# Kernel optimization log

Measured on AMD Instinct MI355X. Metric: run time of the kernel, lower is better.

## Reference

```python
import jax, jax.numpy as jnp
import numpy as np

GC_ALPHA = 3.0  # saturation factor in MTGNN-style graph constructor
TOP_K = 5       # ctor arg: GraphConstructor(n_classes, 5, dim)
EPS_NORM = 1e-12


def setup_inputs() -> dict:
    key = jax.random.key(0)
    k1, k2, k3, k4, k5 = jax.random.split(key, 5)
    B, C, H, W = 32, 384, 80, 80
    N = 27
    return {
        "x": jax.random.normal(k1, (B, C, H, W), dtype=jnp.float32),
        "alpha": jnp.ones((), dtype=jnp.float32),
        "clusters": jax.random.normal(k2, (N, C), dtype=jnp.float32),
        "gc_w1": jax.random.normal(k3, (C, C), dtype=jnp.float32) / np.sqrt(C),
        "gc_w2": jax.random.normal(k4, (C, C), dtype=jnp.float32) / np.sqrt(C),
        "gcn_w": jax.random.normal(k5, (C, C), dtype=jnp.float32) / np.sqrt(C),
    }


def _refine_clusters(clusters, gc_w1, gc_w2, gcn_w):
    # GraphConstructor: learned asymmetric adjacency over n_classes nodes, top-k sparsified
    n = clusters.shape[0]
    a = jnp.tanh(GC_ALPHA * (clusters @ gc_w1))          # [n, d]
    b = jnp.tanh(GC_ALPHA * (clusters @ gc_w2))          # [n, d]
    adj = jax.nn.relu(jnp.tanh(GC_ALPHA * (a @ b.T - b @ a.T)))  # [n, n]
    topv, _ = jax.lax.top_k(adj, TOP_K)
    A = jnp.where(adj >= topv[:, -1:], adj, 0.0)         # keep top-k per row
    # GCNConv (no bias): add self-loops, symmetric normalization
    A_hat = A + jnp.eye(n, dtype=A.dtype)
    dinv = 1.0 / jnp.sqrt(A_hat.sum(axis=1))
    A_norm = dinv[:, None] * A_hat * dinv[None, :]
    return A_norm @ (clusters @ gcn_w)                   # [n, d]


def reference(x, alpha, clusters, gc_w1, gc_w2, gcn_w):
    # mp=True path: refine codebook with tiny GCN over learned graph
    cl = _refine_clusters(clusters, gc_w1, gc_w2, gcn_w)
    # cosine similarity of per-pixel features against codebook
    nc = cl / jnp.maximum(jnp.linalg.norm(cl, axis=1, keepdims=True), EPS_NORM)
    nf = x / jnp.maximum(jnp.linalg.norm(x, axis=1, keepdims=True), EPS_NORM)
    inner_products = jnp.einsum('bchw,nc->bnhw', nf, nc)          # [B, n, H, W]
    cluster_probs = jax.nn.softmax(inner_products * alpha, axis=1)
    cluster_loss = -(cluster_probs * inner_products).sum(axis=1).mean()
    # entropy over unnormalized similarities (computed in original forward)
    p = jax.nn.softmax(jnp.einsum('bchw,nc->bnhw', x, clusters), axis=1)
    entropy = (-(p * jnp.log(p + 1e-10)).sum(axis=1)).mean()
    return cluster_loss, inner_products, cl, entropy
```

## Files before the change

### kernel.cpp

```cpp
#include <hip/hip_runtime.h>
#include <math.h>

#define N_CL   27
#define C_DIM  384
#define HW_SZ  6400
#define B_SZ   32
#define NPIX   (B_SZ*HW_SZ)
#define NTILE  3200
#define NCHUNK 12
#define WSF_PARTS 24576
#define ENT_OFF (1 + (size_t)NPIX*N_CL + (size_t)N_CL*C_DIM)

typedef unsigned short ushort_t;
using bf16x8 = __attribute__((ext_vector_type(8))) short;
using f32x4  = __attribute__((ext_vector_type(4))) float;

__device__ __forceinline__ float xla_tanh_f32(float x) {
    const float c = 7.99881172180175781f;
    if (fabsf(x) < 0.0004f) return x;
    const float xc = fminf(fmaxf(x, -c), c);
    const float x2 = xc*xc;
    float p = fmaf(x2, -2.76076847742355e-16f, 2.00018790482477e-13f);
    p = fmaf(x2, p, -8.60467152213735e-11f);
    p = fmaf(x2, p,  5.12229709037114e-08f);
    p = fmaf(x2, p,  1.48572235717979e-05f);
    p = fmaf(x2, p,  6.37261928875436e-04f);
    p = fmaf(x2, p,  4.89352455891786e-03f);
    p = xc*p;
    float q = fmaf(x2, 1.19825839466702e-06f, 1.18534705686654e-04f);
    q = fmaf(x2, q, 2.26843463243900e-03f);
    q = fmaf(x2, q, 4.89352518554385e-03f);
    return p/q;
}

__global__ __launch_bounds__(384) void cl_refine_mm(const float* __restrict__ clusters,
                                                    const float* __restrict__ w1,
                                                    const float* __restrict__ w2,
                                                    const float* __restrict__ w3,
                                                    float* __restrict__ ws) {
    const int i = blockIdx.x;
    const int m = blockIdx.y;
    const int j = threadIdx.x;
    __shared__ float crow[C_DIM];
    crow[j] = clusters[i*C_DIM + j];
    __syncthreads();
    const float* __restrict__ W = (m==0) ? w1 : (m==1) ? w2 : w3;
    float s0=0.f,s1=0.f,s2=0.f,s3=0.f;
    #pragma unroll 4
    for (int k=0;k<C_DIM;k+=4){
        s0 = fmaf(crow[k+0], W[(size_t)(k+0)*C_DIM + j], s0);
        s1 = fmaf(crow[k+1], W[(size_t)(k+1)*C_DIM + j], s1);
        s2 = fmaf(crow[k+2], W[(size_t)(k+2)*C_DIM + j], s2);
        s3 = fmaf(crow[k+3], W[(size_t)(k+3)*C_DIM + j], s3);
    }
    const float acc = (s0+s1)+(s2+s3);
    ws[(size_t)m*N_CL*C_DIM + i*C_DIM + j] = (m<2) ? xla_tanh_f32(3.0f*acc) : acc;
}

__global__ __launch_bounds__(1024) void cl_adj_graph(float* ws,
                                                     const float* __restrict__ clusters_g,
                                                     float* __restrict__ out) {
    const float* cg = ws + 2*N_CL*C_DIM;
    float* cl_out = out + 1 + (size_t)NPIX*N_CL;
    const int t = threadIdx.x;

    __shared__ float Ash[N_CL][C_DIM+1];
    __shared__ float Bsh[N_CL][C_DIM+1];
    __shared__ float anorm[N_CL][N_CL+1];
    __shared__ float dinv[N_CL];
    __shared__ float rinv[N_CL];
    __shared__ float cls[N_CL][C_DIM];

    for (int idx=t; idx<N_CL*C_DIM; idx+=1024){
        const int i = idx / C_DIM, k = idx - i*C_DIM;
        Ash[i][k] = ws[idx];
        Bsh[i][k] = ws[N_CL*C_DIM + idx];
    }
    __syncthreads();
    if (t < N_CL*N_CL) {
        const int i = t / N_CL, j = t - (t / N_CL)*N_CL;
        float p0=0,p1=0,p2=0,p3=0,q0=0,q1=0,q2=0,q3=0;
        for (int k=0;k<C_DIM;k+=4){
            p0=fmaf(Ash[i][k+0],Bsh[j][k+0],p0); p1=fmaf(Ash[i][k+1],Bsh[j][k+1],p1);
            p2=fmaf(Ash[i][k+2],Bsh[j][k+2],p2); p3=fmaf(Ash[i][k+3],Bsh[j][k+3],p3);
            q0=fmaf(Bsh[i][k+0],Ash[j][k+0],q0); q1=fmaf(Bsh[i][k+1],Ash[j][k+1],q1);
            q2=fmaf(Bsh[i][k+2],Ash[j][k+2],q2); q3=fmaf(Bsh[i][k+3],Ash[j][k+3],q3);
        }
        const float s1v=(p0+p1)+(p2+p3), s2v=(q0+q1)+(q2+q3);
        anorm[i][j] = fmaxf(xla_tanh_f32(3.0f*(s1v-s2v)), 0.f);
    }
    __syncthreads();
    if (t < N_CL) {
        unsigned mask=0; float thr=0.f;
        for (int s=0;s<5;s++){
            float bv=-1.f; int bi2=0;
            for (int j=0;j<N_CL;j++){
                if (mask & (1u<<j)) continue;
                const float v = anorm[t][j];
                if (v > bv){ bv=v; bi2=j; }
            }
            mask |= 1u<<bi2; thr = bv;
        }
        float rs=0.f;
        for (int j=0;j<N_CL;j++){
            float v = anorm[t][j];
            v = (v >= thr) ? v : 0.f;
            if (j==t) v += 1.f;
            anorm[t][j] = v;
            rs += v;
        }
        dinv[t] = 1.0f / sqrtf(rs);
    }
    __syncthreads();
    if (t < N_CL*N_CL) {
        const int i = t / N_CL, j = t - (t / N_CL)*N_CL;
        anorm[i][j] = dinv[i]*anorm[i][j]*dinv[j];
    }
    __syncthreads();
    for (int idx=t; idx<N_CL*C_DIM; idx+=1024){
        const int i = idx / C_DIM, d = idx - i*C_DIM;
        float s=0.f;
        #pragma unroll
        for (int j=0;j<N_CL;j++) s = fmaf(anorm[i][j], cg[(size_t)j*C_DIM + d], s);
        cls[i][d] = s;
        cl_out[idx] = s;
    }
    __syncthreads();
    if (t < N_CL) {
        float ssq=0.f;
        for (int d=0; d<C_DIM; d++){ const float v=cls[t][d]; ssq=fmaf(v,v,ssq); }
        rinv[t] = 1.0f / fmaxf(sqrtf(ssq), 1e-12f);
    }
    __syncthreads();
    ushort_t* wpk = (ushort_t*)ws;
    for (int idx=t; idx<64*C_DIM; idx+=1024){
        const int n = idx / C_DIM, k = idx - n*C_DIM;
        float v = 0.f;
        if (n < N_CL) v = cls[n][k] * rinv[n];
        else if (n >= 32 && n < 32+N_CL) v = clusters_g[(size_t)(n-32)*C_DIM + k];
        const unsigned bits = __float_as_uint(v);
        const ushort_t hi = (ushort_t)(bits >> 16);
        const float lof = v - __uint_as_float(bits & 0xFFFF0000u);
        const ushort_t lo = (ushort_t)(__float_as_uint(lof) >> 16);
        wpk[idx] = hi;
        wpk[64*C_DIM + idx] = lo;
    }
}

__global__ __launch_bounds__(256, 5) void cl_mfma(const float* __restrict__ x,
                                                  const float* __restrict__ alpha_p,
                                                  const ushort_t* __restrict__ wpk,
                                                  float* __restrict__ ws,
                                                  float* __restrict__ out) {
    __shared__ __align__(16) ushort_t lB[2][2][64][40];
    __shared__ float redL[4], redE[4];

    const int tid = threadIdx.x;
    const int blk = blockIdx.x;
    const int b   = blk / 100;
    const int hw0 = (blk - b*100) * 64;
    const float* __restrict__ xb = x + (size_t)b*C_DIM*HW_SZ + hw0;

    const int lane = tid & 63;
    const int w    = tid >> 6;
    const int l15  = lane & 15;
    const int g    = lane >> 4;
    const int k0   = g*8;
    const float* __restrict__ xl = xb + (w*16 + l15);

    const int b_n  = tid >> 2;
    const int b_kb = (tid & 3) * 8;

    uint4 rb0, rb1;
    #define LOADB(c) {                                                            \
        rb0 = *(const uint4*)(wpk + (size_t)(     b_n)*C_DIM + (c)*32 + b_kb);    \
        rb1 = *(const uint4*)(wpk + (size_t)(64 + b_n)*C_DIM + (c)*32 + b_kb); }
    #define WRITEB(bf) {                                                          \
        *(uint4*)(&lB[bf][0][b_n][b_kb]) = rb0;                                   \
        *(uint4*)(&lB[bf][1][b_n][b_kb]) = rb1; }

    #define LOADA(c, S) {                                                         \
        const float* pA = xl + (size_t)((c)*32 + k0)*HW_SZ;                       \
        R##S##0 = pA[0*HW_SZ]; R##S##1 = pA[1*HW_SZ];                             \
        R##S##2 = pA[2*HW_SZ]; R##S##3 = pA[3*HW_SZ];                             \
        R##S##4 = pA[4*HW_SZ]; R##S##5 = pA[5*HW_SZ];                             \
        R##S##6 = pA[6*HW_SZ]; R##S##7 = pA[7*HW_SZ]; }

    union { ushort_t u[8]; bf16x8 v; } Ah;
    float ss = 0.f;
    #define CVT1(e, R) {                                                          \
        Ah.u[e] = (ushort_t)(__float_as_uint(R) >> 16);                           \
        ss = fmaf(R, R, ss); }
    #define CONVERT(S) {                                                          \
        CVT1(0,R##S##0) CVT1(1,R##S##1) CVT1(2,R##S##2) CVT1(3,R##S##3)           \
        CVT1(4,R##S##4) CVT1(5,R##S##5) CVT1(6,R##S##6) CVT1(7,R##S##7) }

    f32x4 acc0={0,0,0,0}, acc1={0,0,0,0}, acc2={0,0,0,0}, acc3={0,0,0,0};
    #define DOMFMA(cur) {                                                         \
        _Pragma("unroll")                                                         \
        for (int t = 0; t < 4; t++) {                                             \
            union { uint4 q; bf16x8 v; } Bh, Bl;                                  \
            Bh.q = *(const uint4*)(&lB[cur][0][t*16 + l15][k0]);                  \
            Bl.q = *(const uint4*)(&lB[cur][1][t*16 + l15][k0]);                  \
            f32x4 a = (t==0)?acc0:(t==1)?acc1:(t==2)?acc2:acc3;                   \
            a = __builtin_amdgcn_mfma_f32_16x16x32_bf16(Ah.v, Bh.v, a, 0,0,0);    \
            a = __builtin_amdgcn_mfma_f32_16x16x32_bf16(Ah.v, Bl.v, a, 0,0,0);    \
            if (t==0) acc0=a; else if (t==1) acc1=a; else if (t==2) acc2=a;       \
            else acc3=a;                                                          \
        } }

    #define KBAR() { asm volatile("s_waitcnt lgkmcnt(0)" ::: "memory");           \
                     __builtin_amdgcn_s_barrier(); }

    float Ra0,Ra1,Ra2,Ra3,Ra4,Ra5,Ra6,Ra7;
    float Rb0,Rb1,Rb2,Rb3,Rb4,Rb5,Rb6,Rb7;
    float Rc0,Rc1,Rc2,Rc3,Rc4,Rc5,Rc6,Rc7;
    float Rd0,Rd1,Rd2,Rd3,Rd4,Rd5,Rd6,Rd7;

    LOADB(0); WRITEB(0);
    LOADB(1);
    LOADA(0, a);
    LOADA(1, b);
    LOADA(2, c);
    LOADA(3, d);
    KBAR();

    #define STEP(cc, S, p) {                                                      \
        CONVERT(S);                                                               \
        DOMFMA(p);                                                                \
        if ((cc)+1 < NCHUNK) WRITEB((p)^1);                                       \
        if ((cc)+2 < NCHUNK) LOADB((cc)+2);                                       \
        if ((cc)+4 < NCHUNK) LOADA((cc)+4, S);                                    \
        if ((cc)+1 < NCHUNK) KBAR(); }

    STEP(0,a,0)  STEP(1,b,1)  STEP(2,c,0)  STEP(3,d,1)
    STEP(4,a,0)  STEP(5,b,1)  STEP(6,c,0)  STEP(7,d,1)
    STEP(8,a,0)  STEP(9,b,1)  STEP(10,c,0) STEP(11,d,1)

    ss += __shfl_xor(ss, 16);
    ss += __shfl_xor(ss, 32);
    f32x4 invv;
    #pragma unroll
    for (int r = 0; r < 4; r++) {
        const float s2 = __shfl(ss, g*4 + r);
        invv[r] = 1.0f / fmaxf(sqrtf(s2), 1e-12f);
    }

    const float alpha = alpha_p[0];
    float* __restrict__ out1 = out + 1;
    const int pxb = hw0 + w*16 + g*4;

    f32x4 st0, st1;
    #pragma unroll
    for (int r=0;r<4;r++){ st0[r] = acc0[r]*invv[r]; st1[r] = acc1[r]*invv[r]; }
    *(f32x4*)(out1 + (size_t)b*N_CL*HW_SZ + (size_t)l15*HW_SZ + pxb) = st0;
    if (l15 <= 10)
        *(f32x4*)(out1 + (size_t)b*N_CL*HW_SZ + (size_t)(16+l15)*HW_SZ + pxb) = st1;

    float wloss = 0.f, went = 0.f;
    #pragma unroll
    for (int r=0;r<4;r++){
        const float ip0 = st0[r], ip1 = st1[r];
        const float v0 = alpha*ip0;
        const float v1 = (l15<=10) ? alpha*ip1 : -INFINITY;
        float mx = fmaxf(v0, v1);
        #pragma unroll
        for (int m=1;m<16;m<<=1) mx = fmaxf(mx, __shfl_xor(mx, m));
        const float e0 = expf(v0 - mx);
        const float e1 = (l15<=10) ? expf(v1 - mx) : 0.f;
        float z = e0 + e1;
        float tt = fmaf(e0, ip0, (l15<=10) ? e1*ip1 : 0.f);
        #pragma unroll
        for (int m=1;m<16;m<<=1){ z += __shfl_xor(z,m); tt += __shfl_xor(tt,m); }
        wloss += tt/z;
        const float c0 = acc2[r];
        const float c1 = (l15<=10) ? acc3[r] : -INFINITY;
        float emx = fmaxf(c0, c1);
        #pragma unroll
        for (int m=1;m<16;m<<=1) emx = fmaxf(emx, __shfl_xor(emx, m));
        const float f0 = expf(c0 - emx);
        const float f1 = (l15<=10) ? expf(c1 - emx) : 0.f;
        float ez = f0 + f1;
        #pragma unroll
        for (int m=1;m<16;m<<=1) ez += __shfl_xor(ez,m);
        const float iz = 1.0f/ez;
        const float p0 = f0*iz, p1 = f1*iz;
        float te = -p0*logf(p0+1e-10f) - p1*logf(p1+1e-10f);
        #pragma unroll
        for (int m=1;m<16;m<<=1) te += __shfl_xor(te,m);
        went += te;
    }
    wloss += __shfl_xor(wloss,16); wloss += __shfl_xor(wloss,32);
    went  += __shfl_xor(went ,16); went  += __shfl_xor(went ,32);
    if (lane == 0) { redL[w] = wloss; redE[w] = went; }
    __syncthreads();
    if (tid == 0) {
        float* parts = ws + WSF_PARTS;
        parts[blk]         = redL[0]+redL[1]+redL[2]+redL[3];
        parts[NTILE + blk] = redE[0]+redE[1]+redE[2]+redE[3];
    }
}

__global__ __launch_bounds__(1024) void cl_final_reduce(const float* __restrict__ ws,
                                                        float* __restrict__ out) {
    __shared__ float r[1024];
    const int t = threadIdx.x;
    const float* parts = ws + WSF_PARTS;
    float s = 0.f;
    for (int j=t; j<NTILE; j+=1024) s += parts[j];
    r[t] = s; __syncthreads();
    for (int sft=512;sft>0;sft>>=1){ if (t<sft) r[t]+=r[t+sft]; __syncthreads(); }
    if (t==0) out[0] = -r[0]*(1.0f/NPIX);
    __syncthreads();
    s = 0.f;
    for (int j=t; j<NTILE; j+=1024) s += parts[NTILE + j];
    r[t] = s; __syncthreads();
    for (int sft=512;sft>0;sft>>=1){ if (t<sft) r[t]+=r[t+sft]; __syncthreads(); }
    if (t==0) out[ENT_OFF] = r[0]*(1.0f/NPIX);
}

extern "C" void kernel_launch(void* const* d_in, const int* in_sizes, int n_in,
                              void* d_out, int out_size, void* d_ws, size_t ws_size,
                              hipStream_t stream) {
    const float* x        = (const float*)d_in[0];
    const float* alpha    = (const float*)d_in[1];
    const float* clusters = (const float*)d_in[2];
    const float* w1       = (const float*)d_in[3];
    const float* w2       = (const float*)d_in[4];
    const float* w3       = (const float*)d_in[5];
    float* out = (float*)d_out;
    float* ws  = (float*)d_ws;

    cl_refine_mm<<<dim3(27,3), dim3(384), 0, stream>>>(clusters, w1, w2, w3, ws);
    cl_adj_graph<<<dim3(1), dim3(1024), 0, stream>>>(ws, clusters, out);
    cl_mfma<<<dim3(NTILE), dim3(256), 0, stream>>>(x, alpha, (const ushort_t*)ws, ws, out);
    cl_final_reduce<<<dim3(1), dim3(1024), 0, stream>>>(ws, out);
}
```

Before: 159.9 us.

## Double pixel tile per block to reuse codebook LDS loads across two fragments

Each block now covers 128 pixels instead of 64, and each wave computes two 16-pixel MFMA fragments that share the same B (codebook) fragments read from LDS. This halves the block count and the per-pixel cost of B staging and barriers. The A prefetch depth drops from four chunks to two chunks across two fragments, and the occupancy hint goes from 5 to 4 waves, which trades latency hiding for more register accumulators.

New measurement: 153.2 us. 4.2% less time.

```diff
diff --git a/kernel.cpp b/kernel.cpp
--- a/kernel.cpp
+++ b/kernel.cpp
@@ -6,7 +6,7 @@
 #define HW_SZ  6400
 #define B_SZ   32
 #define NPIX   (B_SZ*HW_SZ)
-#define NTILE  3200
+#define NTILE  1600
 #define NCHUNK 12
 #define WSF_PARTS 24576
 #define ENT_OFF (1 + (size_t)NPIX*N_CL + (size_t)N_CL*C_DIM)
@@ -147,7 +147,7 @@
     }
 }
 
-__global__ __launch_bounds__(256, 5) void cl_mfma(const float* __restrict__ x,
+__global__ __launch_bounds__(256, 4) void cl_mfma(const float* __restrict__ x,
                                                   const float* __restrict__ alpha_p,
                                                   const ushort_t* __restrict__ wpk,
                                                   float* __restrict__ ws,
@@ -157,8 +157,8 @@
 
     const int tid = threadIdx.x;
     const int blk = blockIdx.x;
-    const int b   = blk / 100;
-    const int hw0 = (blk - b*100) * 64;
+    const int b   = blk / 50;
+    const int hw0 = (blk - b*50) * 128;
     const float* __restrict__ xb = x + (size_t)b*C_DIM*HW_SZ + hw0;
 
     const int lane = tid & 63;
@@ -166,7 +166,8 @@
     const int l15  = lane & 15;
     const int g    = lane >> 4;
     const int k0   = g*8;
-    const float* __restrict__ xl = xb + (w*16 + l15);
+    const float* __restrict__ xl0 = xb + (w*32 + l15);
+    const float* __restrict__ xl1 = xl0 + 16;
 
     const int b_n  = tid >> 2;
     const int b_kb = (tid & 3) * 8;
@@ -179,34 +180,42 @@
         *(uint4*)(&lB[bf][0][b_n][b_kb]) = rb0;                                   \
         *(uint4*)(&lB[bf][1][b_n][b_kb]) = rb1; }
 
-    #define LOADA(c, S) {                                                         \
-        const float* pA = xl + (size_t)((c)*32 + k0)*HW_SZ;                       \
+    #define LOADA(c, S, XL) {                                                     \
+        const float* pA = (XL) + (size_t)((c)*32 + k0)*HW_SZ;                     \
         R##S##0 = pA[0*HW_SZ]; R##S##1 = pA[1*HW_SZ];                             \
         R##S##2 = pA[2*HW_SZ]; R##S##3 = pA[3*HW_SZ];                             \
         R##S##4 = pA[4*HW_SZ]; R##S##5 = pA[5*HW_SZ];                             \
         R##S##6 = pA[6*HW_SZ]; R##S##7 = pA[7*HW_SZ]; }
 
-    union { ushort_t u[8]; bf16x8 v; } Ah;
-    float ss = 0.f;
-    #define CVT1(e, R) {                                                          \
-        Ah.u[e] = (ushort_t)(__float_as_uint(R) >> 16);                           \
-        ss = fmaf(R, R, ss); }
-    #define CONVERT(S) {                                                          \
+    union { ushort_t u[8]; bf16x8 v; } A0h, A1h;
+    float ss0 = 0.f, ss1 = 0.f;
+    #define CVT0(e, R) { A0h.u[e] = (ushort_t)(__float_as_uint(R) >> 16);         \
+                         ss0 = fmaf(R, R, ss0); }
+    #define CVT1(e, R) { A1h.u[e] = (ushort_t)(__float_as_uint(R) >> 16);         \
+                         ss1 = fmaf(R, R, ss1); }
+    #define CONVERT0(S) {                                                         \
+        CVT0(0,R##S##0) CVT0(1,R##S##1) CVT0(2,R##S##2) CVT0(3,R##S##3)           \
+        CVT0(4,R##S##4) CVT0(5,R##S##5) CVT0(6,R##S##6) CVT0(7,R##S##7) }
+    #define CONVERT1(S) {                                                         \
         CVT1(0,R##S##0) CVT1(1,R##S##1) CVT1(2,R##S##2) CVT1(3,R##S##3)           \
         CVT1(4,R##S##4) CVT1(5,R##S##5) CVT1(6,R##S##6) CVT1(7,R##S##7) }
 
-    f32x4 acc0={0,0,0,0}, acc1={0,0,0,0}, acc2={0,0,0,0}, acc3={0,0,0,0};
-    #define DOMFMA(cur) {                                                         \
+    f32x4 acc00={0,0,0,0}, acc01={0,0,0,0}, acc02={0,0,0,0}, acc03={0,0,0,0};
+    f32x4 acc10={0,0,0,0}, acc11={0,0,0,0}, acc12={0,0,0,0}, acc13={0,0,0,0};
+    #define DOCHUNK(p) {                                                          \
         _Pragma("unroll")                                                         \
         for (int t = 0; t < 4; t++) {                                             \
             union { uint4 q; bf16x8 v; } Bh, Bl;                                  \
-            Bh.q = *(const uint4*)(&lB[cur][0][t*16 + l15][k0]);                  \
-            Bl.q = *(const uint4*)(&lB[cur][1][t*16 + l15][k0]);                  \
-            f32x4 a = (t==0)?acc0:(t==1)?acc1:(t==2)?acc2:acc3;                   \
-            a = __builtin_amdgcn_mfma_f32_16x16x32_bf16(Ah.v, Bh.v, a, 0,0,0);    \
-            a = __builtin_amdgcn_mfma_f32_16x16x32_bf16(Ah.v, Bl.v, a, 0,0,0);    \
-            if (t==0) acc0=a; else if (t==1) acc1=a; else if (t==2) acc2=a;       \
-            else acc3=a;                                                          \
+            Bh.q = *(const uint4*)(&lB[p][0][t*16 + l15][k0]);                    \
+            Bl.q = *(const uint4*)(&lB[p][1][t*16 + l15][k0]);                    \
+            f32x4 a0 = (t==0)?acc00:(t==1)?acc01:(t==2)?acc02:acc03;              \
+            f32x4 a1 = (t==0)?acc10:(t==1)?acc11:(t==2)?acc12:acc13;              \
+            a0 = __builtin_amdgcn_mfma_f32_16x16x32_bf16(A0h.v, Bh.v, a0, 0,0,0); \
+            a0 = __builtin_amdgcn_mfma_f32_16x16x32_bf16(A0h.v, Bl.v, a0, 0,0,0); \
+            a1 = __builtin_amdgcn_mfma_f32_16x16x32_bf16(A1h.v, Bh.v, a1, 0,0,0); \
+            a1 = __builtin_amdgcn_mfma_f32_16x16x32_bf16(A1h.v, Bl.v, a1, 0,0,0); \
+            if (t==0){acc00=a0;acc10=a1;} else if (t==1){acc01=a0;acc11=a1;}      \
+            else if (t==2){acc02=a0;acc12=a1;} else {acc03=a0;acc13=a1;}          \
         } }
 
     #define KBAR() { asm volatile("s_waitcnt lgkmcnt(0)" ::: "memory");           \
@@ -219,77 +228,81 @@
 
     LOADB(0); WRITEB(0);
     LOADB(1);
-    LOADA(0, a);
-    LOADA(1, b);
-    LOADA(2, c);
-    LOADA(3, d);
+    LOADA(0, a, xl0); LOADA(0, b, xl1);
+    LOADA(1, c, xl0); LOADA(1, d, xl1);
     KBAR();
 
-    #define STEP(cc, S, p) {                                                      \
-        CONVERT(S);                                                               \
-        DOMFMA(p);                                                                \
+    #define STEP(cc, S0, S1, p) {                                                 \
+        CONVERT0(S0); CONVERT1(S1);                                               \
+        DOCHUNK(p);                                                               \
         if ((cc)+1 < NCHUNK) WRITEB((p)^1);                                       \
-        if ((cc)+2 < NCHUNK) LOADB((cc)+2);                                       \
-        if ((cc)+4 < NCHUNK) LOADA((cc)+4, S);                                    \
+        if ((cc)+2 < NCHUNK) {                                                    \
+            LOADB((cc)+2);                                                        \
+            LOADA((cc)+2, S0, xl0); LOADA((cc)+2, S1, xl1);                       \
+        }                                                                         \
         if ((cc)+1 < NCHUNK) KBAR(); }
 
-    STEP(0,a,0)  STEP(1,b,1)  STEP(2,c,0)  STEP(3,d,1)
-    STEP(4,a,0)  STEP(5,b,1)  STEP(6,c,0)  STEP(7,d,1)
-    STEP(8,a,0)  STEP(9,b,1)  STEP(10,c,0) STEP(11,d,1)
-
-    ss += __shfl_xor(ss, 16);
-    ss += __shfl_xor(ss, 32);
-    f32x4 invv;
-    #pragma unroll
-    for (int r = 0; r < 4; r++) {
-        const float s2 = __shfl(ss, g*4 + r);
-        invv[r] = 1.0f / fmaxf(sqrtf(s2), 1e-12f);
-    }
+    STEP(0,a,b,0)  STEP(1,c,d,1)  STEP(2,a,b,0)  STEP(3,c,d,1)
+    STEP(4,a,b,0)  STEP(5,c,d,1)  STEP(6,a,b,0)  STEP(7,c,d,1)
+    STEP(8,a,b,0)  STEP(9,c,d,1)  STEP(10,a,b,0) STEP(11,c,d,1)
+
+    ss0 += __shfl_xor(ss0, 16); ss0 += __shfl_xor(ss0, 32);
+    ss1 += __shfl_xor(ss1, 16); ss1 += __shfl_xor(ss1, 32);
 
     const float alpha = alpha_p[0];
     float* __restrict__ out1 = out + 1;
-    const int pxb = hw0 + w*16 + g*4;
-
-    f32x4 st0, st1;
-    #pragma unroll
-    for (int r=0;r<4;r++){ st0[r] = acc0[r]*invv[r]; st1[r] = acc1[r]*invv[r]; }
-    *(f32x4*)(out1 + (size_t)b*N_CL*HW_SZ + (size_t)l15*HW_SZ + pxb) = st0;
-    if (l15 <= 10)
-        *(f32x4*)(out1 + (size_t)b*N_CL*HW_SZ + (size_t)(16+l15)*HW_SZ + pxb) = st1;
-
     float wloss = 0.f, went = 0.f;
-    #pragma unroll
-    for (int r=0;r<4;r++){
-        const float ip0 = st0[r], ip1 = st1[r];
-        const float v0 = alpha*ip0;
-        const float v1 = (l15<=10) ? alpha*ip1 : -INFINITY;
-        float mx = fmaxf(v0, v1);
-        #pragma unroll
-        for (int m=1;m<16;m<<=1) mx = fmaxf(mx, __shfl_xor(mx, m));
-        const float e0 = expf(v0 - mx);
-        const float e1 = (l15<=10) ? expf(v1 - mx) : 0.f;
-        float z = e0 + e1;
-        float tt = fmaf(e0, ip0, (l15<=10) ? e1*ip1 : 0.f);
-        #pragma unroll
-        for (int m=1;m<16;m<<=1){ z += __shfl_xor(z,m); tt += __shfl_xor(tt,m); }
-        wloss += tt/z;
-        const float c0 = acc2[r];
-        const float c1 = (l15<=10) ? acc3[r] : -INFINITY;
-        float emx = fmaxf(c0, c1);
-        #pragma unroll
-        for (int m=1;m<16;m<<=1) emx = fmaxf(emx, __shfl_xor(emx, m));
-        const float f0 = expf(c0 - emx);
-        const float f1 = (l15<=10) ? expf(c1 - emx) : 0.f;
-        float ez = f0 + f1;
-        #pragma unroll
-        for (int m=1;m<16;m<<=1) ez += __shfl_xor(ez,m);
-        const float iz = 1.0f/ez;
-        const float p0 = f0*iz, p1 = f1*iz;
-        float te = -p0*logf(p0+1e-10f) - p1*logf(p1+1e-10f);
-        #pragma unroll
-        for (int m=1;m<16;m<<=1) te += __shfl_xor(te,m);
-        went += te;
-    }
+
+    #define EPILOG(F, A0, A1, A2, A3, SS) {                                       \
+        f32x4 invv;                                                               \
+        _Pragma("unroll")                                                         \
+        for (int r = 0; r < 4; r++) {                                             \
+            const float s2 = __shfl(SS, g*4 + r);                                 \
+            invv[r] = 1.0f / fmaxf(sqrtf(s2), 1e-12f);                            \
+        }                                                                         \
+        const int pxb = hw0 + w*32 + (F)*16 + g*4;                                \
+        f32x4 st0, st1;                                                           \
+        _Pragma("unroll")                                                         \
+        for (int r=0;r<4;r++){ st0[r] = A0[r]*invv[r]; st1[r] = A1[r]*invv[r]; }  \
+        *(f32x4*)(out1 + (size_t)b*N_CL*HW_SZ + (size_t)l15*HW_SZ + pxb) = st0;   \
+        if (l15 <= 10)                                                            \
+            *(f32x4*)(out1 + (size_t)b*N_CL*HW_SZ + (size_t)(16+l15)*HW_SZ + pxb) = st1; \
+        _Pragma("unroll")                                                         \
+        for (int r=0;r<4;r++){                                                    \
+            const float ip0 = st0[r], ip1 = st1[r];                               \
+            const float v0 = alpha*ip0;                                           \
+            const float v1 = (l15<=10) ? alpha*ip1 : -INFINITY;                   \
+            float mx = fmaxf(v0, v1);                                             \
+            _Pragma("unroll")                                                     \
+            for (int m=1;m<16;m<<=1) mx = fmaxf(mx, __shfl_xor(mx, m));           \
+            const float e0 = expf(v0 - mx);                                       \
+            const float e1 = (l15<=10) ? expf(v1 - mx) : 0.f;                     \
+            float z = e0 + e1;                                                    \
+            float tt = fmaf(e0, ip0, (l15<=10) ? e1*ip1 : 0.f);                   \
+            _Pragma("unroll")                                                     \
+            for (int m=1;m<16;m<<=1){ z += __shfl_xor(z,m); tt += __shfl_xor(tt,m); } \
+            wloss += tt/z;                                                        \
+            const float c0 = A2[r];                                               \
+            const float c1 = (l15<=10) ? A3[r] : -INFINITY;                       \
+            float emx = fmaxf(c0, c1);                                            \
+            _Pragma("unroll")                                                     \
+            for (int m=1;m<16;m<<=1) emx = fmaxf(emx, __shfl_xor(emx, m));        \
+            const float f0 = expf(c0 - emx);                                      \
+            const float f1 = (l15<=10) ? expf(c1 - emx) : 0.f;                    \
+            float ez = f0 + f1;                                                   \
+            _Pragma("unroll")                                                     \
+            for (int m=1;m<16;m<<=1) ez += __shfl_xor(ez,m);                      \
+            const float iz = 1.0f/ez;                                             \
+            const float p0 = f0*iz, p1 = f1*iz;                                   \
+            float te = -p0*logf(p0+1e-10f) - p1*logf(p1+1e-10f);                  \
+            _Pragma("unroll")                                                     \
+            for (int m=1;m<16;m<<=1) te += __shfl_xor(te,m);                      \
+            went += te;                                                           \
+        } }
+
+    EPILOG(0, acc00, acc01, acc02, acc03, ss0)
+    EPILOG(1, acc10, acc11, acc12, acc13, ss1)
+
     wloss += __shfl_xor(wloss,16); wloss += __shfl_xor(wloss,32);
     went  += __shfl_xor(went ,16); went  += __shfl_xor(went ,32);
     if (lane == 0) { redL[w] = wloss; redE[w] = went; }
```

## Stream x tiles into LDS via global_load_lds with swizzled ring buffer

Applied to the files above, without the earlier changes.

Replaces per-thread scalar strided global loads of x into registers with 16-byte direct global-to-LDS loads. These fill a 4-slot ring of 32-channel chunks with an XOR swizzle, and each thread then reads its 8 channel values from LDS for the bf16 MFMA. The B-matrix prefetch is reorganised into two register sets, and the loop is re-pipelined with a lookahead of three chunks. The aim is wider, better-coalesced reads of the large x tensor and lower register pressure. The cost is extra LDS, with occupancy bounds dropped from 5 to 3 blocks per CU, and correctness relies on the async LDS writes being complete before they are read.

New measurement: 159.0 us. Within noise of the previous version (-0.6%).

```diff
diff --git a/kernel.cpp b/kernel.cpp
--- a/kernel.cpp
+++ b/kernel.cpp
@@ -147,11 +147,12 @@
     }
 }
 
-__global__ __launch_bounds__(256, 5) void cl_mfma(const float* __restrict__ x,
+__global__ __launch_bounds__(256, 3) void cl_mfma(const float* __restrict__ x,
                                                   const float* __restrict__ alpha_p,
                                                   const ushort_t* __restrict__ wpk,
                                                   float* __restrict__ ws,
                                                   float* __restrict__ out) {
+    __shared__ __align__(16) float lA[4*2048];
     __shared__ __align__(16) ushort_t lB[2][2][64][40];
     __shared__ float redL[4], redE[4];
 
@@ -166,34 +167,42 @@
     const int l15  = lane & 15;
     const int g    = lane >> 4;
     const int k0   = g*8;
-    const float* __restrict__ xl = xb + (w*16 + l15);
+    const int pxsw = (w*16 + l15) ^ (g << 4);
+
+    const float* gA = xb + ((size_t)(w*8 + (lane >> 4)) * HW_SZ
+                            + (((lane & 15) * 4) ^ (w << 4)));
 
     const int b_n  = tid >> 2;
     const int b_kb = (tid & 3) * 8;
 
-    uint4 rb0, rb1;
-    #define LOADB(c) {                                                            \
-        rb0 = *(const uint4*)(wpk + (size_t)(     b_n)*C_DIM + (c)*32 + b_kb);    \
-        rb1 = *(const uint4*)(wpk + (size_t)(64 + b_n)*C_DIM + (c)*32 + b_kb); }
-    #define WRITEB(bf) {                                                          \
-        *(uint4*)(&lB[bf][0][b_n][b_kb]) = rb0;                                   \
-        *(uint4*)(&lB[bf][1][b_n][b_kb]) = rb1; }
-
-    #define LOADA(c, S) {                                                         \
-        const float* pA = xl + (size_t)((c)*32 + k0)*HW_SZ;                       \
-        R##S##0 = pA[0*HW_SZ]; R##S##1 = pA[1*HW_SZ];                             \
-        R##S##2 = pA[2*HW_SZ]; R##S##3 = pA[3*HW_SZ];                             \
-        R##S##4 = pA[4*HW_SZ]; R##S##5 = pA[5*HW_SZ];                             \
-        R##S##6 = pA[6*HW_SZ]; R##S##7 = pA[7*HW_SZ]; }
+    uint4 rbA0, rbA1;
+    uint4 rbB0, rbB1;
+    #define LOADB_S0(c) {                                                         \
+        rbA0 = *(const uint4*)(wpk + (size_t)(     b_n)*C_DIM + (c)*32 + b_kb);   \
+        rbA1 = *(const uint4*)(wpk + (size_t)(64 + b_n)*C_DIM + (c)*32 + b_kb); }
+    #define LOADB_S1(c) {                                                         \
+        rbB0 = *(const uint4*)(wpk + (size_t)(     b_n)*C_DIM + (c)*32 + b_kb);   \
+        rbB1 = *(const uint4*)(wpk + (size_t)(64 + b_n)*C_DIM + (c)*32 + b_kb); }
+    #define WRITEB_S0() {                                                         \
+        *(uint4*)(&lB[0][0][b_n][b_kb]) = rbA0;                                   \
+        *(uint4*)(&lB[0][1][b_n][b_kb]) = rbA1; }
+    #define WRITEB_S1() {                                                         \
+        *(uint4*)(&lB[1][0][b_n][b_kb]) = rbB0;                                   \
+        *(uint4*)(&lB[1][1][b_n][b_kb]) = rbB1; }
+
+    #define GLLA(c) {                                                             \
+        const float* g0 = gA + (size_t)((c)*32) * HW_SZ;                          \
+        float* l0 = lA + (size_t)((c) & 3) * 2048 + (size_t)(w*8) * 64;           \
+        __builtin_amdgcn_global_load_lds(                                         \
+            (const __attribute__((address_space(1))) void*)g0,                    \
+            (__attribute__((address_space(3))) void*)l0, 16, 0, 0);               \
+        __builtin_amdgcn_global_load_lds(                                         \
+            (const __attribute__((address_space(1))) void*)(g0 + (size_t)4*HW_SZ),\
+            (__attribute__((address_space(3))) void*)(l0 + 4*64), 16, 0, 0);      \
+    }
 
     union { ushort_t u[8]; bf16x8 v; } Ah;
     float ss = 0.f;
-    #define CVT1(e, R) {                                                          \
-        Ah.u[e] = (ushort_t)(__float_as_uint(R) >> 16);                           \
-        ss = fmaf(R, R, ss); }
-    #define CONVERT(S) {                                                          \
-        CVT1(0,R##S##0) CVT1(1,R##S##1) CVT1(2,R##S##2) CVT1(3,R##S##3)           \
-        CVT1(4,R##S##4) CVT1(5,R##S##5) CVT1(6,R##S##6) CVT1(7,R##S##7) }
 
     f32x4 acc0={0,0,0,0}, acc1={0,0,0,0}, acc2={0,0,0,0}, acc3={0,0,0,0};
     #define DOMFMA(cur) {                                                         \
@@ -212,30 +221,29 @@
     #define KBAR() { asm volatile("s_waitcnt lgkmcnt(0)" ::: "memory");           \
                      __builtin_amdgcn_s_barrier(); }
 
-    float Ra0,Ra1,Ra2,Ra3,Ra4,Ra5,Ra6,Ra7;
-    float Rb0,Rb1,Rb2,Rb3,Rb4,Rb5,Rb6,Rb7;
-    float Rc0,Rc1,Rc2,Rc3,Rc4,Rc5,Rc6,Rc7;
-    float Rd0,Rd1,Rd2,Rd3,Rd4,Rd5,Rd6,Rd7;
-
-    LOADB(0); WRITEB(0);
-    LOADB(1);
-    LOADA(0, a);
-    LOADA(1, b);
-    LOADA(2, c);
-    LOADA(3, d);
+    GLLA(0); LOADB_S0(0);
+    GLLA(1); LOADB_S1(1);
+    WRITEB_S0();
+    GLLA(2); LOADB_S0(2);
     KBAR();
 
-    #define STEP(cc, S, p) {                                                      \
-        CONVERT(S);                                                               \
-        DOMFMA(p);                                                                \
-        if ((cc)+1 < NCHUNK) WRITEB((p)^1);                                       \
-        if ((cc)+2 < NCHUNK) LOADB((cc)+2);                                       \
-        if ((cc)+4 < NCHUNK) LOADA((cc)+4, S);                                    \
-        if ((cc)+1 < NCHUNK) KBAR(); }
-
-    STEP(0,a,0)  STEP(1,b,1)  STEP(2,c,0)  STEP(3,d,1)
-    STEP(4,a,0)  STEP(5,b,1)  STEP(6,c,0)  STEP(7,d,1)
-    STEP(8,a,0)  STEP(9,b,1)  STEP(10,c,0) STEP(11,d,1)
+    #pragma unroll
+    for (int c = 0; c < NCHUNK; ++c) {
+        if (c + 1 < NCHUNK) { if ((c+1) & 1) { WRITEB_S1(); } else { WRITEB_S0(); } }
+        if (c + 3 < NCHUNK) GLLA(c+3);
+        {
+            const float* lAc = lA + (size_t)(c & 3) * 2048;
+            #pragma unroll
+            for (int e = 0; e < 8; ++e) {
+                const float v = lAc[(size_t)(k0 + e) * 64 + pxsw];
+                Ah.u[e] = (ushort_t)(__float_as_uint(v) >> 16);
+                ss = fmaf(v, v, ss);
+            }
+            if (c & 1) { DOMFMA(1); } else { DOMFMA(0); }
+        }
+        if (c + 3 < NCHUNK) { if ((c+3) & 1) { LOADB_S1(c+3); } else { LOADB_S0(c+3); } }
+        if (c + 1 < NCHUNK) KBAR();
+    }
 
     ss += __shfl_xor(ss, 16);
     ss += __shfl_xor(ss, 32);
```
